# Kernel tuning notes

Measured on AMD Instinct MI355X. Metric: run time of the kernel, lower is better.

## Reference

```python
import jax, jax.numpy as jnp
import numpy as np

HEADS = 8
DIM_HEAD = 64
SCALE = DIM_HEAD ** -0.5


def setup_inputs() -> dict:
    key = jax.random.key(0)
    k1, k2, k3 = jax.random.split(key, 3)
    B, N, D = 4, 2048, HEADS * DIM_HEAD  # D = inner_dim = 512
    x = jax.random.normal(k1, (B, N, D), dtype=jnp.float32)
    # nn.Linear weights stored transposed vs torch; here we use [in, out]
    w_qkv = jax.random.normal(k2, (D, 3 * D), dtype=jnp.float32) * (D ** -0.5)
    w_out = jax.random.normal(k3, (D, D), dtype=jnp.float32) * (D ** -0.5)
    b_out = jnp.zeros((D,), dtype=jnp.float32)
    return {"x": x, "w_qkv": w_qkv, "w_out": w_out, "b_out": b_out}


def reference(x, w_qkv, w_out, b_out):
    B, N, D = x.shape
    qkv = x @ w_qkv  # [B, N, 3D]
    q, k, v = jnp.split(qkv, 3, axis=-1)

    def to_heads(t):  # b n (h d) -> b h n d
        return t.reshape(B, N, HEADS, DIM_HEAD).transpose(0, 2, 1, 3)

    q, k, v = to_heads(q), to_heads(k), to_heads(v)
    dots = jnp.einsum('bhnd,bhmd->bhnm', q, k) * SCALE  # [B,H,N,N]
    attn = jax.nn.softmax(dots, axis=-1)
    out = jnp.einsum('bhnm,bhmd->bhnd', attn, v)  # [B,H,N,d]
    out = out.transpose(0, 2, 1, 3).reshape(B, N, D)  # b h n d -> b n (h d)
    return out @ w_out + b_out
```

## Files before the change

### kernel.cpp

```cpp
#include <hip/hip_runtime.h>

typedef __bf16 bf16;
typedef __bf16 bf16x8 __attribute__((ext_vector_type(8)));
typedef __bf16 bf16x4 __attribute__((ext_vector_type(4)));
typedef float f32x4 __attribute__((ext_vector_type(4)));
typedef float f32x16 __attribute__((ext_vector_type(16)));

#define MFMA16(a, b, c) __builtin_amdgcn_mfma_f32_16x16x32_bf16(a, b, c, 0, 0, 0)
#define MFMA32(a, b, c) __builtin_amdgcn_mfma_f32_32x32x16_bf16(a, b, c, 0, 0, 0)

#define CS 0.18033688011112042f

#if __has_builtin(__builtin_amdgcn_exp2f)
#define EXP2(x) __builtin_amdgcn_exp2f(x)
#else
#define EXP2(x) exp2f(x)
#endif

#define WAIT_VM0() __builtin_amdgcn_s_waitcnt(0x0F70)
#define WAIT_VM8() __builtin_amdgcn_s_waitcnt(0x0F78)

__device__ __forceinline__ void load_lds16(const bf16* g, bf16* l) {
    __builtin_amdgcn_global_load_lds(
        (const __attribute__((address_space(1))) unsigned int*)g,
        (__attribute__((address_space(3))) unsigned int*)l, 16, 0, 0);
}

__device__ __forceinline__ bf16x4 shfl_xor32_b64(bf16x4 v) {
    union { bf16x4 b; int i[2]; } u;
    u.b = v;
    u.i[0] = __shfl_xor(u.i[0], 32, 64);
    u.i[1] = __shfl_xor(u.i[1], 32, 64);
    return u.b;
}

__device__ __forceinline__ bf16x8 build_bfrag(bf16x4 plo, bf16x4 phi, int h) {
    bf16x4 xlo = shfl_xor32_b64(plo);
    bf16x4 xhi = shfl_xor32_b64(phi);
    bf16x4 lo4 = h ? xhi : plo;
    bf16x4 hi4 = h ? phi : xlo;
    bf16x8 bb;
#pragma unroll
    for (int i = 0; i < 4; ++i) { bb[i] = lo4[i]; bb[4 + i] = hi4[i]; }
    return bb;
}

__global__ __launch_bounds__(256) void f32_to_bf16_kernel(const float* __restrict__ in,
                                                          bf16* __restrict__ out, int n) {
    int i = (blockIdx.x * 256 + threadIdx.x) * 4;
    if (i < n) {
        float4 v = *(const float4*)&in[i];
        bf16x4 o = {(bf16)v.x, (bf16)v.y, (bf16)v.z, (bf16)v.w};
        *(bf16x4*)&out[i] = o;
    }
}

__global__ __launch_bounds__(256) void transpose_f2b(const float* __restrict__ in,
                                                     bf16* __restrict__ out,
                                                     int R, int C) {
    __shared__ float tile[32][33];
    int tx = threadIdx.x & 31, ty = threadIdx.x >> 5;
    int c0 = blockIdx.x * 32, r0 = blockIdx.y * 32;
#pragma unroll
    for (int i = ty; i < 32; i += 8)
        tile[i][tx] = in[(size_t)(r0 + i) * C + c0 + tx];
    __syncthreads();
#pragma unroll
    for (int i = ty; i < 32; i += 8)
        out[(size_t)(c0 + i) * R + r0 + tx] = (bf16)tile[tx][i];
}

__global__ __launch_bounds__(256) void transpose_v_kernel(const bf16* __restrict__ qkv,
                                                          bf16* __restrict__ vt) {
    __shared__ bf16 tile[32][33];
    int tx = threadIdx.x & 31, ty = threadIdx.x >> 5;
    int bh = blockIdx.z, b = bh >> 3, h = bh & 7;
    int n0 = blockIdx.x * 32, d0 = blockIdx.y * 32;
#pragma unroll
    for (int i = ty; i < 32; i += 8)
        tile[i][tx] = qkv[(size_t)(b * 2048 + n0 + i) * 1536 + 1024 + h * 64 + d0 + tx];
    __syncthreads();
#pragma unroll
    for (int i = ty; i < 32; i += 8)
        vt[(size_t)(bh * 64 + d0 + i) * 2048 + n0 + tx] = tile[tx][i];
}

template <int MT, int MODE, typename OutT>
__global__ __launch_bounds__(256, (MT == 4) ? 2 : 4)
void gemm_bt_kernel(const bf16* __restrict__ A,
                    const bf16* __restrict__ Bt,
                    const float* __restrict__ bias,
                    OutT* __restrict__ C,
                    int M, int N, int K) {
    const int BM = MT * 32;
    __shared__ bf16 As[BM * 64];
    __shared__ bf16 Bs[128 * 64];
    int t = threadIdx.x;
    int lane = t & 63, w = t >> 6;
    int wr = w >> 1, wc = w & 1;
    int quad = lane >> 4, r16 = lane & 15;
    int m0 = blockIdx.y * BM, n0 = blockIdx.x * 128;

    const f32x4 fzero = {0.f, 0.f, 0.f, 0.f};
    f32x4 acc[MT][4];
#pragma unroll
    for (int i = 0; i < MT; ++i)
#pragma unroll
        for (int j = 0; j < 4; ++j) acc[i][j] = fzero;

    const bf16* ap[MT]; bf16* ad[MT];
    const bf16* bp[4];  bf16* bd[4];
#pragma unroll
    for (int i = 0; i < MT; ++i) {
        int ci = i * 256 + t;
        int row = ci >> 3, cp = ci & 7, cc = cp ^ (row & 7);
        ap[i] = &A[(size_t)(m0 + row) * K + cc * 8];
        ad[i] = &As[ci * 8];
    }
#pragma unroll
    for (int i = 0; i < 4; ++i) {
        int ci = i * 256 + t;
        int row = ci >> 3, cp = ci & 7, cc = cp ^ (row & 7);
        bp[i] = &Bt[(size_t)(n0 + row) * K + cc * 8];
        bd[i] = &Bs[ci * 8];
    }

    for (int k0 = 0; k0 < K; k0 += 64) {
        __syncthreads();
#pragma unroll
        for (int i = 0; i < MT; ++i) { load_lds16(ap[i], ad[i]); ap[i] += 64; }
#pragma unroll
        for (int i = 0; i < 4; ++i) { load_lds16(bp[i], bd[i]); bp[i] += 64; }
        __syncthreads();
#pragma unroll
        for (int ks = 0; ks < 2; ++ks) {
            bf16x8 af[MT], bfr[4];
            int cp = (ks * 4 + quad) ^ (r16 & 7);
#pragma unroll
            for (int mt = 0; mt < MT; ++mt)
                af[mt] = *(const bf16x8*)&As[(wr * (BM / 2) + mt * 16 + r16) * 64 + cp * 8];
#pragma unroll
            for (int nt = 0; nt < 4; ++nt)
                bfr[nt] = *(const bf16x8*)&Bs[(wc * 64 + nt * 16 + r16) * 64 + cp * 8];
#pragma unroll
            for (int mt = 0; mt < MT; ++mt)
#pragma unroll
                for (int nt = 0; nt < 4; ++nt)
                    acc[mt][nt] = MFMA16(af[mt], bfr[nt], acc[mt][nt]);
        }
    }
#pragma unroll
    for (int mt = 0; mt < MT; ++mt)
#pragma unroll
        for (int nt = 0; nt < 4; ++nt)
#pragma unroll
            for (int r = 0; r < 4; ++r) {
                int row = m0 + wr * (BM / 2) + mt * 16 + quad * 4 + r;
                int col = n0 + wc * 64 + nt * 16 + r16;
                float v = acc[mt][nt][r];
                if (MODE == 1 && n0 < 512) v *= CS;
                if (MODE == 2) v += bias[col];
                C[(size_t)row * N + col] = (OutT)v;
            }
}

__global__ __launch_bounds__(128, 2) void attn_kernel(const bf16* __restrict__ qkv,
                                                      const bf16* __restrict__ vt,
                                                      bf16* __restrict__ out) {
    __shared__ __align__(16) char smemraw[32768];
    bf16* stage = (bf16*)smemraw;

    int t = threadIdx.x;
    int lane = t & 63, w = t >> 6;
    int h = lane >> 5, q = lane & 31;
    int bh = blockIdx.y, b = bh >> 3, hd = bh & 7;
    int qb = blockIdx.x * 64;

    bf16x8 qf[2][4];
#pragma unroll
    for (int sub = 0; sub < 2; ++sub) {
        size_t qoff = (size_t)(b * 2048 + qb + sub * 32 + q) * 1536 + hd * 64;
#pragma unroll
        for (int s = 0; s < 4; ++s)
            qf[sub][s] = *(const bf16x8*)&qkv[qoff + s * 16 + h * 8];
    }

    f32x16 o_acc[2][2];
#pragma unroll
    for (int sub = 0; sub < 2; ++sub)
#pragma unroll
        for (int db = 0; db < 2; ++db)
#pragma unroll
            for (int i = 0; i < 16; ++i) o_acc[sub][db][i] = 0.f;
    float psum[2] = {0.f, 0.f};

    bf16* base = stage + w * 8192;

    const bf16* kp[4]; const bf16* vp[4];
    int kdo[4], vdo[4];
#pragma unroll
    for (int rdd = 0; rdd < 4; ++rdd) {
        int ciK = rdd * 64 + lane;
        int rowK = ciK >> 3, ccK = (ciK & 7) ^ (rowK & 7);
        kp[rdd] = &qkv[(size_t)(b * 2048 + w * 1024 + rowK) * 1536 + 512 + hd * 64 + ccK * 8];
        kdo[rdd] = ciK * 8;
        int ciV = rdd * 64 + lane;
        int rowV = ciV >> 2, ccV = (ciV & 3) ^ (rowV & 3);
        vp[rdd] = &vt[(size_t)(bh * 64 + rowV) * 2048 + w * 1024 + ccV * 8];
        vdo[rdd] = 2048 + ciV * 8;
    }

#pragma unroll
    for (int rdd = 0; rdd < 4; ++rdd) {
        load_lds16(kp[rdd], base + kdo[rdd]);  kp[rdd] += (size_t)32 * 1536;
        load_lds16(vp[rdd], base + vdo[rdd]);  vp[rdd] += 32;
    }

    for (int it = 0; it < 32; ++it) {
        const bf16* Ks = base + (it & 1) * 4096;
        const bf16* Vs = Ks + 2048;
        if (it < 31) {
            bf16* nb = base + ((it + 1) & 1) * 4096;
#pragma unroll
            for (int rdd = 0; rdd < 4; ++rdd) {
                load_lds16(kp[rdd], nb + kdo[rdd]);  kp[rdd] += (size_t)32 * 1536;
                load_lds16(vp[rdd], nb + vdo[rdd]);  vp[rdd] += 32;
            }
            WAIT_VM8();
        } else {
            WAIT_VM0();
        }

        bf16x8 kf[4];
#pragma unroll
        for (int s = 0; s < 4; ++s) {
            int cp = (s * 2 + h) ^ (q & 7);
            kf[s] = *(const bf16x8*)&Ks[q * 64 + cp * 8];
        }
        bf16x8 vf[2][2];
#pragma unroll
        for (int kstep = 0; kstep < 2; ++kstep)
#pragma unroll
            for (int db = 0; db < 2; ++db) {
                int cp = (kstep * 2 + h) ^ (q & 3);
                vf[kstep][db] = *(const bf16x8*)&Vs[(db * 32 + q) * 32 + cp * 8];
            }

#pragma unroll
        for (int sub = 0; sub < 2; ++sub) {
            f32x16 sacc;
#pragma unroll
            for (int i = 0; i < 16; ++i) sacc[i] = 0.f;
#pragma unroll
            for (int s = 0; s < 4; ++s)
                sacc = MFMA32(kf[s], qf[sub][s], sacc);

            bf16x4 pk[4];
            float ps = 0.f;
#pragma unroll
            for (int g8 = 0; g8 < 4; ++g8)
#pragma unroll
                for (int i = 0; i < 4; ++i) {
                    float p = EXP2(sacc[4 * g8 + i]);
                    ps += p;
                    pk[g8][i] = (bf16)p;
                }
            psum[sub] += ps;
            bf16x8 bfr0 = build_bfrag(pk[0], pk[1], h);
            bf16x8 bfr1 = build_bfrag(pk[2], pk[3], h);

#pragma unroll
            for (int db = 0; db < 2; ++db) {
                o_acc[sub][db] = MFMA32(vf[0][db], bfr0, o_acc[sub][db]);
                o_acc[sub][db] = MFMA32(vf[1][db], bfr1, o_acc[sub][db]);
            }
        }
    }

    float l_own[2];
#pragma unroll
    for (int sub = 0; sub < 2; ++sub)
        l_own[sub] = psum[sub] + __shfl_xor(psum[sub], 32, 64);

    __syncthreads();
    float* Of = (float*)smemraw;
    float* Lf = (float*)(smemraw + 17408);

    if (w == 1) {
#pragma unroll
        for (int sub = 0; sub < 2; ++sub) {
#pragma unroll
            for (int db = 0; db < 2; ++db)
#pragma unroll
                for (int r = 0; r < 16; ++r) {
                    int d = db * 32 + (r & 3) + 8 * (r >> 2) + 4 * h;
                    Of[(sub * 32 + q) * 68 + d] = o_acc[sub][db][r];
                }
            if (h == 0) Lf[sub * 32 + q] = l_own[sub];
        }
    }
    __syncthreads();
    if (w == 0) {
#pragma unroll
        for (int sub = 0; sub < 2; ++sub) {
#pragma unroll
            for (int db = 0; db < 2; ++db)
#pragma unroll
                for (int r = 0; r < 16; ++r) {
                    int d = db * 32 + (r & 3) + 8 * (r >> 2) + 4 * h;
                    Of[(sub * 32 + q) * 68 + d] += o_acc[sub][db][r];
                }
            if (h == 0) Lf[sub * 32 + q] += l_own[sub];
        }
    }
    __syncthreads();

    {
        int row = t >> 1, half = t & 1;
        float linv = 1.f / Lf[row];
        const float* src = &Of[row * 68 + half * 32];
        bf16* dst = &out[(size_t)(b * 2048 + qb + row) * 512 + hd * 64 + half * 32];
#pragma unroll
        for (int i = 0; i < 4; ++i) {
            f32x4 a = *(const f32x4*)&src[i * 8];
            f32x4 c = *(const f32x4*)&src[i * 8 + 4];
            bf16x8 o8;
#pragma unroll
            for (int j = 0; j < 4; ++j) {
                o8[j] = (bf16)(a[j] * linv);
                o8[4 + j] = (bf16)(c[j] * linv);
            }
            *(bf16x8*)&dst[i * 8] = o8;
        }
    }
}

extern "C" void kernel_launch(void* const* d_in, const int* in_sizes, int n_in,
                              void* d_out, int out_size, void* d_ws, size_t ws_size,
                              hipStream_t stream) {
    const float* x     = (const float*)d_in[0];
    const float* w_qkv = (const float*)d_in[1];
    const float* w_out = (const float*)d_in[2];
    const float* b_out = (const float*)d_in[3];
    float* out = (float*)d_out;

    char* ws = (char*)d_ws;
    size_t off = 0;
    bf16* xb    = (bf16*)(ws + off); off += (size_t)8192 * 512 * 2;
    bf16* wqkvT = (bf16*)(ws + off); off += (size_t)1536 * 512 * 2;
    bf16* woutT = (bf16*)(ws + off); off += (size_t)512 * 512 * 2;
    bf16* qkv   = (bf16*)(ws + off); off += (size_t)8192 * 1536 * 2;
    bf16* vt    = (bf16*)(ws + off); off += (size_t)32 * 64 * 2048 * 2;
    bf16* attn  = (bf16*)(ws + off);

    f32_to_bf16_kernel<<<4096, 256, 0, stream>>>(x, xb, 8192 * 512);
    transpose_f2b<<<dim3(48, 16), 256, 0, stream>>>(w_qkv, wqkvT, 512, 1536);
    transpose_f2b<<<dim3(16, 16), 256, 0, stream>>>(w_out, woutT, 512, 512);
    gemm_bt_kernel<4, 1, bf16><<<dim3(12, 64), 256, 0, stream>>>(
        xb, wqkvT, nullptr, qkv, 8192, 1536, 512);
    transpose_v_kernel<<<dim3(64, 2, 32), 256, 0, stream>>>(qkv, vt);
    attn_kernel<<<dim3(32, 32), 128, 0, stream>>>(qkv, vt, attn);
    gemm_bt_kernel<2, 2, float><<<dim3(4, 128), 256, 0, stream>>>(
        attn, woutT, b_out, out, 8192, 512, 512);
}
```

Measured before the change: 167.2 us.

## Split attention across four waves sharing one cooperatively loaded K/V tile

The attention kernel moves from 2 waves, each streaming its own half of the keys into private LDS buffers for 64 queries, to 4 waves. The 4 waves split as 2 query halves by 2 key halves and share a block-wide 64-key K/V double buffer. All threads load that buffer cooperatively, with a barrier per iteration. The aim is to cut per-wave register use, raise occupancy, and stop the two query subtiles from each reloading K/V fragments. It also adds s_setprio around the MFMA groups, at the cost of two block barriers per key step.

Measured after the change: 168.1 us. Within noise of the previous version (+0.6%).

```diff
diff --git a/kernel.cpp b/kernel.cpp
--- a/kernel.cpp
+++ b/kernel.cpp
@@ -18,7 +18,10 @@
 #endif
 
 #define WAIT_VM0() __builtin_amdgcn_s_waitcnt(0x0F70)
-#define WAIT_VM8() __builtin_amdgcn_s_waitcnt(0x0F78)
+#define WAIT_VM4() __builtin_amdgcn_s_waitcnt(0x0F74)
+
+#define BARRIER() __builtin_amdgcn_s_barrier()
+#define CFENCE() asm volatile("" ::: "memory")
 
 __device__ __forceinline__ void load_lds16(const bf16* g, bf16* l) {
     __builtin_amdgcn_global_load_lds(
@@ -164,7 +167,7 @@
             }
 }
 
-__global__ __launch_bounds__(128, 2) void attn_kernel(const bf16* __restrict__ qkv,
+__global__ __launch_bounds__(256, 4) void attn_kernel(const bf16* __restrict__ qkv,
                                                       const bf16* __restrict__ vt,
                                                       bf16* __restrict__ out) {
     __shared__ __align__(16) char smemraw[32768];
@@ -172,156 +175,145 @@
 
     int t = threadIdx.x;
     int lane = t & 63, w = t >> 6;
+    int wq = w & 1, wk = w >> 1;
     int h = lane >> 5, q = lane & 31;
     int bh = blockIdx.y, b = bh >> 3, hd = bh & 7;
     int qb = blockIdx.x * 64;
 
-    bf16x8 qf[2][4];
-#pragma unroll
-    for (int sub = 0; sub < 2; ++sub) {
-        size_t qoff = (size_t)(b * 2048 + qb + sub * 32 + q) * 1536 + hd * 64;
+    bf16x8 qf[4];
+    {
+        size_t qoff = (size_t)(b * 2048 + qb + wq * 32 + q) * 1536 + hd * 64;
 #pragma unroll
         for (int s = 0; s < 4; ++s)
-            qf[sub][s] = *(const bf16x8*)&qkv[qoff + s * 16 + h * 8];
-    }
-
-    f32x16 o_acc[2][2];
-#pragma unroll
-    for (int sub = 0; sub < 2; ++sub)
-#pragma unroll
-        for (int db = 0; db < 2; ++db)
-#pragma unroll
-            for (int i = 0; i < 16; ++i) o_acc[sub][db][i] = 0.f;
-    float psum[2] = {0.f, 0.f};
-
-    bf16* base = stage + w * 8192;
-
-    const bf16* kp[4]; const bf16* vp[4];
-    int kdo[4], vdo[4];
-#pragma unroll
-    for (int rdd = 0; rdd < 4; ++rdd) {
-        int ciK = rdd * 64 + lane;
-        int rowK = ciK >> 3, ccK = (ciK & 7) ^ (rowK & 7);
-        kp[rdd] = &qkv[(size_t)(b * 2048 + w * 1024 + rowK) * 1536 + 512 + hd * 64 + ccK * 8];
-        kdo[rdd] = ciK * 8;
-        int ciV = rdd * 64 + lane;
-        int rowV = ciV >> 2, ccV = (ciV & 3) ^ (rowV & 3);
-        vp[rdd] = &vt[(size_t)(bh * 64 + rowV) * 2048 + w * 1024 + ccV * 8];
-        vdo[rdd] = 2048 + ciV * 8;
-    }
-
-#pragma unroll
-    for (int rdd = 0; rdd < 4; ++rdd) {
-        load_lds16(kp[rdd], base + kdo[rdd]);  kp[rdd] += (size_t)32 * 1536;
-        load_lds16(vp[rdd], base + vdo[rdd]);  vp[rdd] += 32;
+            qf[s] = *(const bf16x8*)&qkv[qoff + s * 16 + h * 8];
+    }
+
+    f32x16 o_acc[2];
+#pragma unroll
+    for (int db = 0; db < 2; ++db)
+#pragma unroll
+        for (int i = 0; i < 16; ++i) o_acc[db][i] = 0.f;
+    float psum = 0.f;
+
+    const bf16* kp[2]; const bf16* vp[2];
+    int kdo[2], vdo[2];
+#pragma unroll
+    for (int j = 0; j < 2; ++j) {
+        int ci = j * 256 + t;
+        int row = ci >> 3, cp = ci & 7, cc = cp ^ (row & 7);
+        kp[j] = &qkv[(size_t)(b * 2048 + row) * 1536 + 512 + hd * 64 + cc * 8];
+        kdo[j] = ci * 8;
+        vp[j] = &vt[(size_t)(bh * 64 + row) * 2048 + cc * 8];
+        vdo[j] = 4096 + ci * 8;
+    }
+
+#pragma unroll
+    for (int j = 0; j < 2; ++j) {
+        load_lds16(kp[j], stage + kdo[j]);  kp[j] += (size_t)64 * 1536;
+        load_lds16(vp[j], stage + vdo[j]);  vp[j] += 64;
     }
 
     for (int it = 0; it < 32; ++it) {
-        const bf16* Ks = base + (it & 1) * 4096;
-        const bf16* Vs = Ks + 2048;
+        const bf16* Ks = stage + (it & 1) * 8192;
+        const bf16* Vs = Ks + 4096;
         if (it < 31) {
-            bf16* nb = base + ((it + 1) & 1) * 4096;
-#pragma unroll
-            for (int rdd = 0; rdd < 4; ++rdd) {
-                load_lds16(kp[rdd], nb + kdo[rdd]);  kp[rdd] += (size_t)32 * 1536;
-                load_lds16(vp[rdd], nb + vdo[rdd]);  vp[rdd] += 32;
-            }
-            WAIT_VM8();
+            bf16* nb = stage + ((it + 1) & 1) * 8192;
+#pragma unroll
+            for (int j = 0; j < 2; ++j) {
+                load_lds16(kp[j], nb + kdo[j]);  kp[j] += (size_t)64 * 1536;
+                load_lds16(vp[j], nb + vdo[j]);  vp[j] += 64;
+            }
+            WAIT_VM4();
         } else {
             WAIT_VM0();
         }
+        CFENCE(); BARRIER(); CFENCE();
 
         bf16x8 kf[4];
 #pragma unroll
         for (int s = 0; s < 4; ++s) {
             int cp = (s * 2 + h) ^ (q & 7);
-            kf[s] = *(const bf16x8*)&Ks[q * 64 + cp * 8];
+            kf[s] = *(const bf16x8*)&Ks[(wk * 32 + q) * 64 + cp * 8];
         }
         bf16x8 vf[2][2];
 #pragma unroll
         for (int kstep = 0; kstep < 2; ++kstep)
 #pragma unroll
             for (int db = 0; db < 2; ++db) {
-                int cp = (kstep * 2 + h) ^ (q & 3);
-                vf[kstep][db] = *(const bf16x8*)&Vs[(db * 32 + q) * 32 + cp * 8];
-            }
-
-#pragma unroll
-        for (int sub = 0; sub < 2; ++sub) {
-            f32x16 sacc;
-#pragma unroll
-            for (int i = 0; i < 16; ++i) sacc[i] = 0.f;
-#pragma unroll
-            for (int s = 0; s < 4; ++s)
-                sacc = MFMA32(kf[s], qf[sub][s], sacc);
-
-            bf16x4 pk[4];
-            float ps = 0.f;
-#pragma unroll
-            for (int g8 = 0; g8 < 4; ++g8)
-#pragma unroll
-                for (int i = 0; i < 4; ++i) {
-                    float p = EXP2(sacc[4 * g8 + i]);
-                    ps += p;
-                    pk[g8][i] = (bf16)p;
-                }
-            psum[sub] += ps;
-            bf16x8 bfr0 = build_bfrag(pk[0], pk[1], h);
-            bf16x8 bfr1 = build_bfrag(pk[2], pk[3], h);
-
-#pragma unroll
-            for (int db = 0; db < 2; ++db) {
-                o_acc[sub][db] = MFMA32(vf[0][db], bfr0, o_acc[sub][db]);
-                o_acc[sub][db] = MFMA32(vf[1][db], bfr1, o_acc[sub][db]);
-            }
-        }
-    }
-
-    float l_own[2];
-#pragma unroll
-    for (int sub = 0; sub < 2; ++sub)
-        l_own[sub] = psum[sub] + __shfl_xor(psum[sub], 32, 64);
+                int cp = (wk * 4 + kstep * 2 + h) ^ (q & 7);
+                vf[kstep][db] = *(const bf16x8*)&Vs[(db * 32 + q) * 64 + cp * 8];
+            }
+
+        f32x16 sacc;
+#pragma unroll
+        for (int i = 0; i < 16; ++i) sacc[i] = 0.f;
+        __builtin_amdgcn_s_setprio(1);
+#pragma unroll
+        for (int s = 0; s < 4; ++s)
+            sacc = MFMA32(kf[s], qf[s], sacc);
+        __builtin_amdgcn_s_setprio(0);
+
+        bf16x4 pk[4];
+        float ps = 0.f;
+#pragma unroll
+        for (int g8 = 0; g8 < 4; ++g8)
+#pragma unroll
+            for (int i = 0; i < 4; ++i) {
+                float p = EXP2(sacc[4 * g8 + i]);
+                ps += p;
+                pk[g8][i] = (bf16)p;
+            }
+        psum += ps;
+        bf16x8 bfr0 = build_bfrag(pk[0], pk[1], h);
+        bf16x8 bfr1 = build_bfrag(pk[2], pk[3], h);
+
+        __builtin_amdgcn_s_setprio(1);
+#pragma unroll
+        for (int db = 0; db < 2; ++db) {
+            o_acc[db] = MFMA32(vf[0][db], bfr0, o_acc[db]);
+            o_acc[db] = MFMA32(vf[1][db], bfr1, o_acc[db]);
+        }
+        __builtin_amdgcn_s_setprio(0);
+
+        CFENCE(); BARRIER(); CFENCE();
+    }
+
+    float l_own = psum + __shfl_xor(psum, 32, 64);
 
     __syncthreads();
     float* Of = (float*)smemraw;
     float* Lf = (float*)(smemraw + 17408);
 
-    if (w == 1) {
-#pragma unroll
-        for (int sub = 0; sub < 2; ++sub) {
-#pragma unroll
-            for (int db = 0; db < 2; ++db)
-#pragma unroll
-                for (int r = 0; r < 16; ++r) {
-                    int d = db * 32 + (r & 3) + 8 * (r >> 2) + 4 * h;
-                    Of[(sub * 32 + q) * 68 + d] = o_acc[sub][db][r];
-                }
-            if (h == 0) Lf[sub * 32 + q] = l_own[sub];
-        }
-    }
-    __syncthreads();
-    if (w == 0) {
-#pragma unroll
-        for (int sub = 0; sub < 2; ++sub) {
-#pragma unroll
-            for (int db = 0; db < 2; ++db)
-#pragma unroll
-                for (int r = 0; r < 16; ++r) {
-                    int d = db * 32 + (r & 3) + 8 * (r >> 2) + 4 * h;
-                    Of[(sub * 32 + q) * 68 + d] += o_acc[sub][db][r];
-                }
-            if (h == 0) Lf[sub * 32 + q] += l_own[sub];
-        }
+    if (wk == 1) {
+#pragma unroll
+        for (int db = 0; db < 2; ++db)
+#pragma unroll
+            for (int r = 0; r < 16; ++r) {
+                int d = db * 32 + (r & 3) + 8 * (r >> 2) + 4 * h;
+                Of[(wq * 32 + q) * 68 + d] = o_acc[db][r];
+            }
+        if (h == 0) Lf[wq * 32 + q] = l_own;
+    }
+    __syncthreads();
+    if (wk == 0) {
+#pragma unroll
+        for (int db = 0; db < 2; ++db)
+#pragma unroll
+            for (int r = 0; r < 16; ++r) {
+                int d = db * 32 + (r & 3) + 8 * (r >> 2) + 4 * h;
+                Of[(wq * 32 + q) * 68 + d] += o_acc[db][r];
+            }
+        if (h == 0) Lf[wq * 32 + q] += l_own;
     }
     __syncthreads();
 
     {
-        int row = t >> 1, half = t & 1;
+        int row = t >> 2, qt = t & 3;
         float linv = 1.f / Lf[row];
-        const float* src = &Of[row * 68 + half * 32];
-        bf16* dst = &out[(size_t)(b * 2048 + qb + row) * 512 + hd * 64 + half * 32];
-#pragma unroll
-        for (int i = 0; i < 4; ++i) {
+        const float* src = &Of[row * 68 + qt * 16];
+        bf16* dst = &out[(size_t)(b * 2048 + qb + row) * 512 + hd * 64 + qt * 16];
+#pragma unroll
+        for (int i = 0; i < 2; ++i) {
             f32x4 a = *(const f32x4*)&src[i * 8];
             f32x4 c = *(const f32x4*)&src[i * 8 + 4];
             bf16x8 o8;
@@ -359,7 +351,7 @@
     gemm_bt_kernel<4, 1, bf16><<<dim3(12, 64), 256, 0, stream>>>(
         xb, wqkvT, nullptr, qkv, 8192, 1536, 512);
     transpose_v_kernel<<<dim3(64, 2, 32), 256, 0, stream>>>(qkv, vt);
-    attn_kernel<<<dim3(32, 32), 128, 0, stream>>>(qkv, vt, attn);
+    attn_kernel<<<dim3(32, 32), 256, 0, stream>>>(qkv, vt, attn);
     gemm_bt_kernel<2, 2, float><<<dim3(4, 128), 256, 0, stream>>>(
         attn, woutT, b_out, out, 8192, 512, 512);
 }
```

## Load K/V fragments directly from global into registers, dropping LDS staging

Applied to the files above, without the earlier changes.

Replaces the async global-to-LDS double-buffered staging of K and V tiles with direct per-lane global loads into register fragments, ping-ponged across two register sets so loads for the next tile overlap compute of the current one. Shared memory shrinks to what the final cross-wave reduction needs, and the exp/sum loop is split into four independent accumulators. This removes LDS writes and reads plus the explicit waitcnt, but each lane now issues uncoalesced 16-byte global loads (K rows strided by 1536 elements) and depends on cache hits and compiler-inserted waits. Register pressure also rises from holding two fragment sets.

After: 183.2 us. +9.6%, slower.

```diff
diff --git a/kernel.cpp b/kernel.cpp
--- a/kernel.cpp
+++ b/kernel.cpp
@@ -16,9 +16,6 @@
 #else
 #define EXP2(x) exp2f(x)
 #endif
-
-#define WAIT_VM0() __builtin_amdgcn_s_waitcnt(0x0F70)
-#define WAIT_VM8() __builtin_amdgcn_s_waitcnt(0x0F78)
 
 __device__ __forceinline__ void load_lds16(const bf16* g, bf16* l) {
     __builtin_amdgcn_global_load_lds(
@@ -164,11 +161,62 @@
             }
 }
 
+struct KVFrags {
+    bf16x8 kf[4];
+    bf16x8 vf[2][2];
+};
+
+__device__ __forceinline__ void load_frags(KVFrags& f, const bf16* kb,
+                                           const bf16* vb0, const bf16* vb1) {
+#pragma unroll
+    for (int s = 0; s < 4; ++s)
+        f.kf[s] = *(const bf16x8*)(kb + s * 16);
+#pragma unroll
+    for (int kstep = 0; kstep < 2; ++kstep) {
+        f.vf[kstep][0] = *(const bf16x8*)(vb0 + kstep * 16);
+        f.vf[kstep][1] = *(const bf16x8*)(vb1 + kstep * 16);
+    }
+}
+
+__device__ __forceinline__ void compute_tile(const KVFrags& f, const bf16x8 (&qf)[2][4],
+                                             f32x16 (&o_acc)[2][2], float (&psum)[2], int h) {
+#pragma unroll
+    for (int sub = 0; sub < 2; ++sub) {
+        f32x16 sacc;
+#pragma unroll
+        for (int i = 0; i < 16; ++i) sacc[i] = 0.f;
+#pragma unroll
+        for (int s = 0; s < 4; ++s)
+            sacc = MFMA32(f.kf[s], qf[sub][s], sacc);
+
+        bf16x4 pk[4];
+        float ps0 = 0.f, ps1 = 0.f, ps2 = 0.f, ps3 = 0.f;
+#pragma unroll
+        for (int i = 0; i < 4; ++i) {
+            float p0 = EXP2(sacc[i]);
+            float p1 = EXP2(sacc[4 + i]);
+            float p2 = EXP2(sacc[8 + i]);
+            float p3 = EXP2(sacc[12 + i]);
+            ps0 += p0; ps1 += p1; ps2 += p2; ps3 += p3;
+            pk[0][i] = (bf16)p0; pk[1][i] = (bf16)p1;
+            pk[2][i] = (bf16)p2; pk[3][i] = (bf16)p3;
+        }
+        psum[sub] += (ps0 + ps1) + (ps2 + ps3);
+        bf16x8 bfr0 = build_bfrag(pk[0], pk[1], h);
+        bf16x8 bfr1 = build_bfrag(pk[2], pk[3], h);
+
+#pragma unroll
+        for (int db = 0; db < 2; ++db) {
+            o_acc[sub][db] = MFMA32(f.vf[0][db], bfr0, o_acc[sub][db]);
+            o_acc[sub][db] = MFMA32(f.vf[1][db], bfr1, o_acc[sub][db]);
+        }
+    }
+}
+
 __global__ __launch_bounds__(128, 2) void attn_kernel(const bf16* __restrict__ qkv,
                                                       const bf16* __restrict__ vt,
                                                       bf16* __restrict__ out) {
-    __shared__ __align__(16) char smemraw[32768];
-    bf16* stage = (bf16*)smemraw;
+    __shared__ __align__(16) char smemraw[17664];
 
     int t = threadIdx.x;
     int lane = t & 63, w = t >> 6;
@@ -194,88 +242,27 @@
             for (int i = 0; i < 16; ++i) o_acc[sub][db][i] = 0.f;
     float psum[2] = {0.f, 0.f};
 
-    bf16* base = stage + w * 8192;
-
-    const bf16* kp[4]; const bf16* vp[4];
-    int kdo[4], vdo[4];
-#pragma unroll
-    for (int rdd = 0; rdd < 4; ++rdd) {
-        int ciK = rdd * 64 + lane;
-        int rowK = ciK >> 3, ccK = (ciK & 7) ^ (rowK & 7);
-        kp[rdd] = &qkv[(size_t)(b * 2048 + w * 1024 + rowK) * 1536 + 512 + hd * 64 + ccK * 8];
-        kdo[rdd] = ciK * 8;
-        int ciV = rdd * 64 + lane;
-        int rowV = ciV >> 2, ccV = (ciV & 3) ^ (rowV & 3);
-        vp[rdd] = &vt[(size_t)(bh * 64 + rowV) * 2048 + w * 1024 + ccV * 8];
-        vdo[rdd] = 2048 + ciV * 8;
-    }
-
-#pragma unroll
-    for (int rdd = 0; rdd < 4; ++rdd) {
-        load_lds16(kp[rdd], base + kdo[rdd]);  kp[rdd] += (size_t)32 * 1536;
-        load_lds16(vp[rdd], base + vdo[rdd]);  vp[rdd] += 32;
-    }
-
-    for (int it = 0; it < 32; ++it) {
-        const bf16* Ks = base + (it & 1) * 4096;
-        const bf16* Vs = Ks + 2048;
-        if (it < 31) {
-            bf16* nb = base + ((it + 1) & 1) * 4096;
-#pragma unroll
-            for (int rdd = 0; rdd < 4; ++rdd) {
-                load_lds16(kp[rdd], nb + kdo[rdd]);  kp[rdd] += (size_t)32 * 1536;
-                load_lds16(vp[rdd], nb + vdo[rdd]);  vp[rdd] += 32;
-            }
-            WAIT_VM8();
-        } else {
-            WAIT_VM0();
-        }
-
-        bf16x8 kf[4];
-#pragma unroll
-        for (int s = 0; s < 4; ++s) {
-            int cp = (s * 2 + h) ^ (q & 7);
-            kf[s] = *(const bf16x8*)&Ks[q * 64 + cp * 8];
-        }
-        bf16x8 vf[2][2];
-#pragma unroll
-        for (int kstep = 0; kstep < 2; ++kstep)
-#pragma unroll
-            for (int db = 0; db < 2; ++db) {
-                int cp = (kstep * 2 + h) ^ (q & 3);
-                vf[kstep][db] = *(const bf16x8*)&Vs[(db * 32 + q) * 32 + cp * 8];
-            }
-
-#pragma unroll
-        for (int sub = 0; sub < 2; ++sub) {
-            f32x16 sacc;
-#pragma unroll
-            for (int i = 0; i < 16; ++i) sacc[i] = 0.f;
-#pragma unroll
-            for (int s = 0; s < 4; ++s)
-                sacc = MFMA32(kf[s], qf[sub][s], sacc);
-
-            bf16x4 pk[4];
-            float ps = 0.f;
-#pragma unroll
-            for (int g8 = 0; g8 < 4; ++g8)
-#pragma unroll
-                for (int i = 0; i < 4; ++i) {
-                    float p = EXP2(sacc[4 * g8 + i]);
-                    ps += p;
-                    pk[g8][i] = (bf16)p;
-                }
-            psum[sub] += ps;
-            bf16x8 bfr0 = build_bfrag(pk[0], pk[1], h);
-            bf16x8 bfr1 = build_bfrag(pk[2], pk[3], h);
-
-#pragma unroll
-            for (int db = 0; db < 2; ++db) {
-                o_acc[sub][db] = MFMA32(vf[0][db], bfr0, o_acc[sub][db]);
-                o_acc[sub][db] = MFMA32(vf[1][db], bfr1, o_acc[sub][db]);
-            }
-        }
-    }
+    const bf16* kb  = &qkv[(size_t)(b * 2048 + w * 1024 + q) * 1536 + 512 + hd * 64 + h * 8];
+    const bf16* vb0 = &vt[(size_t)(bh * 64 + q) * 2048 + w * 1024 + h * 8];
+    const bf16* vb1 = &vt[(size_t)(bh * 64 + 32 + q) * 2048 + w * 1024 + h * 8];
+    const size_t KSTEP = (size_t)32 * 1536;
+
+    KVFrags fA, fB;
+    load_frags(fA, kb, vb0, vb1);
+    kb += KSTEP; vb0 += 32; vb1 += 32;
+
+#pragma unroll 1
+    for (int it2 = 0; it2 < 15; ++it2) {
+        load_frags(fB, kb, vb0, vb1);
+        kb += KSTEP; vb0 += 32; vb1 += 32;
+        compute_tile(fA, qf, o_acc, psum, h);
+        load_frags(fA, kb, vb0, vb1);
+        kb += KSTEP; vb0 += 32; vb1 += 32;
+        compute_tile(fB, qf, o_acc, psum, h);
+    }
+    load_frags(fB, kb, vb0, vb1);
+    compute_tile(fA, qf, o_acc, psum, h);
+    compute_tile(fB, qf, o_acc, psum, h);
 
     float l_own[2];
 #pragma unroll
```
